# Optimization experiments

Hardware: AMD Instinct MI355X
Metric: run time of the kernel (lower is better)

The kernel has to match this reference:

```python
import jax, jax.numpy as jnp
import numpy as np

N, E, D, H = 100000, 600000, 128, 256
BN_EPS = 1e-5


def setup_inputs() -> dict:
    key = jax.random.key(0)
    ks = jax.random.split(key, 6)
    node_rep = jax.random.normal(ks[0], (N, D), dtype=jnp.float32)
    edge_attr = jax.random.normal(ks[1], (E, D), dtype=jnp.float32)
    src = jax.random.randint(ks[2], (E,), 0, N)
    dst = jax.random.randint(ks[3], (E,), 0, N)
    ones_e = jnp.ones((E,), dtype=jnp.float32)
    degree = jax.ops.segment_sum(ones_e, src, num_segments=N) + \
             jax.ops.segment_sum(ones_e, dst, num_segments=N)
    eps = jnp.zeros((1,), dtype=jnp.float32)
    W1 = jax.random.normal(ks[4], (H, D), dtype=jnp.float32) * 0.05
    W2 = jax.random.normal(ks[5], (D, H), dtype=jnp.float32) * 0.05
    g1 = jnp.ones((H,), dtype=jnp.float32)
    b1 = jnp.zeros((H,), dtype=jnp.float32)
    g2 = jnp.ones((D,), dtype=jnp.float32)
    b2 = jnp.zeros((D,), dtype=jnp.float32)
    return {"node_rep": node_rep, "edge_attr": edge_attr, "degree": degree,
            "eps": eps, "W1": W1, "g1": g1, "b1": b1,
            "W2": W2, "g2": g2, "b2": b2, "src": src, "dst": dst}


def _bn_relu(x, gamma, beta):
    # BatchNorm1d training mode: batch mean, biased variance
    mu = jnp.mean(x, axis=0)
    var = jnp.mean(jnp.square(x - mu), axis=0)
    return jax.nn.relu((x - mu) * jax.lax.rsqrt(var + BN_EPS) * gamma + beta)


def reference(node_rep, edge_attr, degree, eps, W1, g1, b1, W2, g2, b2, src, dst):
    n = node_rep.shape[0]
    # gather nodes -> edges (sum of two endpoint features), add edge attributes
    m = node_rep[src] + node_rep[dst] + edge_attr            # [E, D]
    # gather edges -> nodes (sum over incident edges)
    node_new = jax.ops.segment_sum(m, src, num_segments=n) + \
               jax.ops.segment_sum(m, dst, num_segments=n)  # [N, D]
    # degree-scaled residual: node_new + (1 + eps - deg) * node_rep
    h = node_new + (1.0 + eps - degree[:, None]) * node_rep  # [N, D]
    # 2-layer MLP: Linear(no bias) -> BN -> ReLU, twice
    h = _bn_relu(jnp.einsum('nd,hd->nh', h, W1), g1, b1)     # [N, H]
    out = _bn_relu(jnp.einsum('nh,dh->nd', h, W2), g2, b2)   # [N, D]
    return out
```

## Files before the change

kernel.cpp:

```cpp
#include <hip/hip_runtime.h>
#include <stdint.h>

#define D 128
#define H 256
#define LSTR 264

typedef short s8v __attribute__((ext_vector_type(8)));
typedef float f4v __attribute__((ext_vector_type(4)));

__device__ __forceinline__ short f2bf(float f){
  union { float f; unsigned u; } v; v.f = f;
  unsigned r = v.u + 0x7fffu + ((v.u >> 16) & 1u);
  return (short)(r >> 16);
}

__global__ void k_prep(const float* __restrict__ W1, const float* __restrict__ W2,
                       short* __restrict__ W1s, short* __restrict__ W2s,
                       float* __restrict__ st1, float* __restrict__ st2,
                       int* __restrict__ counts, int N_){
  int t = blockIdx.x*256 + threadIdx.x;
  if (t < 32768){
    int j = t & 7, lane = (t>>3) & 63, kt = (t>>9) & 3, jt = t>>11;
    int col = jt*16 + (lane & 15);
    int k   = kt*32 + (lane>>4)*8 + j;
    W1s[t] = f2bf(W1[col*D + k]);
  } else if (t < 65536){
    int u = t - 32768;
    int j = u & 7, lane = (u>>3) & 63, kt = (u>>9) & 7, jt = u>>12;
    int col = jt*16 + (lane & 15);
    int k   = kt*32 + (lane>>4)*8 + j;
    W2s[u] = f2bf(W2[col*H + k]);
  } else if (t < 90112){
    int u = t - 65536;
    if (u < 32*2*H) st1[u] = 0.f;
    else st2[u - 32*2*H] = 0.f;
  } else {
    int u = t - 90112;
    if (u <= N_) counts[u] = 0;
  }
}

__global__ void k_count(const int* __restrict__ src, const int* __restrict__ dst,
                        int* __restrict__ counts, int E_){
  int e = blockIdx.x*256 + threadIdx.x;
  if (e >= E_) return;
  atomicAdd(&counts[src[e]], 1);
  atomicAdd(&counts[dst[e]], 1);
}

__global__ void k_scanA(const int* __restrict__ counts, int* __restrict__ blockSums, int N_){
  int t = threadIdx.x;
  int base = blockIdx.x*1024 + t*4;
  int s = 0;
  if (base + 3 < N_){
    int4 v = *(const int4*)(counts + base);
    s = v.x + v.y + v.z + v.w;
  } else {
    for (int i=0;i<4;i++) if (base+i < N_) s += counts[base+i];
  }
  __shared__ int ws4[4];
  for (int o=1; o<64; o<<=1) s += __shfl_xor(s, o);
  if ((t & 63) == 0) ws4[t>>6] = s;
  __syncthreads();
  if (t == 0) blockSums[blockIdx.x] = ws4[0]+ws4[1]+ws4[2]+ws4[3];
}

__global__ void k_scanB(const int* __restrict__ blockSums, int* __restrict__ blockBase,
                        int* __restrict__ offsets, int nb, int N_){
  __shared__ int part[1024];
  int t = threadIdx.x;
  int v = (t < nb) ? blockSums[t] : 0;
  part[t] = v;
  __syncthreads();
  for (int o=1; o<1024; o<<=1){
    int u = (t >= o) ? part[t-o] : 0;
    __syncthreads();
    part[t] += u;
    __syncthreads();
  }
  if (t < nb) blockBase[t] = part[t] - v;
  if (t == nb-1) offsets[N_] = part[t];
}

__global__ void k_scanC(const int* __restrict__ counts, const int* __restrict__ blockBase,
                        int* __restrict__ offsets, int* __restrict__ cursor, int N_){
  __shared__ int part[256];
  int t = threadIdx.x;
  int base = blockIdx.x*1024 + t*4;
  int c[4]; int s = 0;
#pragma unroll
  for (int i=0;i<4;i++){ c[i] = (base+i < N_) ? counts[base+i] : 0; s += c[i]; }
  part[t] = s;
  __syncthreads();
  for (int o=1; o<256; o<<=1){
    int u = (t >= o) ? part[t-o] : 0;
    __syncthreads();
    part[t] += u;
    __syncthreads();
  }
  int pos = blockBase[blockIdx.x] + part[t] - s;
#pragma unroll
  for (int i=0;i<4;i++){
    if (base+i < N_){ offsets[base+i] = pos; cursor[base+i] = pos; pos += c[i]; }
  }
}

__global__ void k_fill(const int* __restrict__ src, const int* __restrict__ dst,
                       int* __restrict__ cursor, int* __restrict__ entries, int E_){
  int e = blockIdx.x*256 + threadIdx.x;
  if (e >= E_) return;
  int p = atomicAdd(&cursor[src[e]], 1);
  entries[p] = (e<<1) | 1;
  int q = atomicAdd(&cursor[dst[e]], 1);
  entries[q] = (e<<1);
}

__global__ void k_gather(const float* __restrict__ x, const float* __restrict__ ea,
                         const int* __restrict__ src, const int* __restrict__ dst,
                         const int* __restrict__ offsets, const int* __restrict__ entries,
                         const float* __restrict__ eps, float* __restrict__ h, int N_){
  int n = (blockIdx.x*256 + threadIdx.x) >> 6;
  int lane = threadIdx.x & 63;
  if (n >= N_) return;
  int lo = offsets[n], hi = offsets[n+1];
  float2 xr = ((const float2*)(x + (size_t)n*D))[lane];
  float sc = 1.0f + eps[0];
  float ax = sc*xr.x, ay = sc*xr.y;
  for (int base = lo; base < hi; base += 64){
    int cnt = min(64, hi - base);
    int ent = 0, oth = 0;
    if (lane < cnt){
      ent = entries[base + lane];
      int e = ent >> 1;
      oth = (ent & 1) ? dst[e] : src[e];
    }
    int j = 0;
    for (; j+3 < cnt; j += 4){
      int e0 = __shfl(ent, j)   >> 1, o0 = __shfl(oth, j);
      int e1 = __shfl(ent, j+1) >> 1, o1 = __shfl(oth, j+1);
      int e2 = __shfl(ent, j+2) >> 1, o2 = __shfl(oth, j+2);
      int e3 = __shfl(ent, j+3) >> 1, o3 = __shfl(oth, j+3);
      float2 m0 = ((const float2*)(ea + (size_t)e0*D))[lane];
      float2 x0 = ((const float2*)(x  + (size_t)o0*D))[lane];
      float2 m1 = ((const float2*)(ea + (size_t)e1*D))[lane];
      float2 x1 = ((const float2*)(x  + (size_t)o1*D))[lane];
      float2 m2 = ((const float2*)(ea + (size_t)e2*D))[lane];
      float2 x2 = ((const float2*)(x  + (size_t)o2*D))[lane];
      float2 m3 = ((const float2*)(ea + (size_t)e3*D))[lane];
      float2 x3 = ((const float2*)(x  + (size_t)o3*D))[lane];
      ax += (m0.x + x0.x) + (m1.x + x1.x) + (m2.x + x2.x) + (m3.x + x3.x);
      ay += (m0.y + x0.y) + (m1.y + x1.y) + (m2.y + x2.y) + (m3.y + x3.y);
    }
    for (; j < cnt; j++){
      int e0 = __shfl(ent, j) >> 1, o0 = __shfl(oth, j);
      float2 m0 = ((const float2*)(ea + (size_t)e0*D))[lane];
      float2 x0 = ((const float2*)(x  + (size_t)o0*D))[lane];
      ax += m0.x + x0.x;
      ay += m0.y + x0.y;
    }
  }
  float2 o; o.x = ax; o.y = ay;
  ((float2*)(h + (size_t)n*D))[lane] = o;
}

__global__ void k_gemm1(const float* __restrict__ h, const short* __restrict__ W1s,
                        float* __restrict__ st1, int nW){
  int wid = (blockIdx.x*256 + threadIdx.x) >> 6;
  int lane = threadIdx.x & 63;
  if (wid >= nW) return;
  int r0 = wid*16;
  int mrow = lane & 15, kg = lane >> 4;
  const float* hrow = h + (size_t)(r0 + mrow)*D + kg*8;
  s8v af[4];
#pragma unroll
  for (int kt=0; kt<4; kt++){
    float4 v0 = *(const float4*)(hrow + kt*32);
    float4 v1 = *(const float4*)(hrow + kt*32 + 4);
    s8v a;
    a[0]=f2bf(v0.x); a[1]=f2bf(v0.y); a[2]=f2bf(v0.z); a[3]=f2bf(v0.w);
    a[4]=f2bf(v1.x); a[5]=f2bf(v1.y); a[6]=f2bf(v1.z); a[7]=f2bf(v1.w);
    af[kt] = a;
  }
  const s8v* Bf = (const s8v*)W1s;
  int shadow = wid & 31;
#pragma unroll
  for (int jt=0; jt<16; jt++){
    f4v acc = {0.f,0.f,0.f,0.f};
#pragma unroll
    for (int kt=0; kt<4; kt++)
      acc = __builtin_amdgcn_mfma_f32_16x16x32_bf16(af[kt], Bf[(jt*4+kt)*64 + lane], acc, 0, 0, 0);
    float s = 0.f, q = 0.f;
#pragma unroll
    for (int r=0; r<4; r++){ s += acc[r]; q += acc[r]*acc[r]; }
    s += __shfl_xor(s, 16); s += __shfl_xor(s, 32);
    q += __shfl_xor(q, 16); q += __shfl_xor(q, 32);
    if (lane < 16){
      atomicAdd(&st1[shadow*(2*H) + jt*16 + lane], s);
      atomicAdd(&st1[shadow*(2*H) + H + jt*16 + lane], q);
    }
  }
}

__global__ void k_fin1(const float* __restrict__ st1, const float* __restrict__ g,
                       const float* __restrict__ b, float* __restrict__ a,
                       float* __restrict__ c, float invN){
  int j = threadIdx.x;
  float s=0.f, q=0.f;
  for (int i=0;i<32;i++){ s += st1[i*(2*H) + j]; q += st1[i*(2*H) + H + j]; }
  float mu = s*invN;
  float var = q*invN - mu*mu;
  float rs = rsqrtf(var + 1e-5f);
  float aa = g[j]*rs;
  a[j] = aa; c[j] = b[j] - mu*aa;
}

__launch_bounds__(256)
__global__ void k_gemm2(const float* __restrict__ h, const short* __restrict__ W1s,
                        const short* __restrict__ W2s,
                        const float* __restrict__ a1, const float* __restrict__ c1,
                        float* __restrict__ Y2, float* __restrict__ st2, int nW){
  __shared__ short P[4*16*LSTR];
  int wib  = threadIdx.x >> 6;
  int lane = threadIdx.x & 63;
  int wid  = blockIdx.x*4 + wib;
  bool valid = wid < nW;
  int r0 = wid*16;
  int mrow = lane & 15, kg = lane >> 4;
  short* Pw = P + wib*16*LSTR;

  s8v af[4];
#pragma unroll
  for (int kt=0; kt<4; kt++){ s8v z = {0,0,0,0,0,0,0,0}; af[kt] = z; }
  if (valid){
    const float* hrow = h + (size_t)(r0 + mrow)*D + kg*8;
#pragma unroll
    for (int kt=0; kt<4; kt++){
      float4 v0 = *(const float4*)(hrow + kt*32);
      float4 v1 = *(const float4*)(hrow + kt*32 + 4);
      s8v a;
      a[0]=f2bf(v0.x); a[1]=f2bf(v0.y); a[2]=f2bf(v0.z); a[3]=f2bf(v0.w);
      a[4]=f2bf(v1.x); a[5]=f2bf(v1.y); a[6]=f2bf(v1.z); a[7]=f2bf(v1.w);
      af[kt] = a;
    }
  }

  const s8v* B1 = (const s8v*)W1s;
#pragma unroll
  for (int jt=0; jt<16; jt++){
    f4v acc = {0.f,0.f,0.f,0.f};
#pragma unroll
    for (int kt=0; kt<4; kt++)
      acc = __builtin_amdgcn_mfma_f32_16x16x32_bf16(af[kt], B1[(jt*4+kt)*64 + lane], acc, 0, 0, 0);
    int col = jt*16 + mrow;
    float a = a1[col], c = c1[col];
#pragma unroll
    for (int r=0; r<4; r++){
      float e = fmaxf(acc[r]*a + c, 0.f);
      Pw[(kg*4 + r)*LSTR + col] = f2bf(e);
    }
  }
  __syncthreads();

  s8v af2[8];
#pragma unroll
  for (int kt2=0; kt2<8; kt2++)
    af2[kt2] = *(const s8v*)(Pw + mrow*LSTR + kt2*32 + kg*8);

  const s8v* B2 = (const s8v*)W2s;
  int shadow = wid & 31;
#pragma unroll
  for (int jt=0; jt<8; jt++){
    f4v acc = {0.f,0.f,0.f,0.f};
#pragma unroll
    for (int kt2=0; kt2<8; kt2++)
      acc = __builtin_amdgcn_mfma_f32_16x16x32_bf16(af2[kt2], B2[(jt*8+kt2)*64 + lane], acc, 0, 0, 0);
    float s=0.f, q=0.f;
    if (valid){
#pragma unroll
      for (int r=0; r<4; r++){
        int row = r0 + kg*4 + r;
        Y2[(size_t)row*D + jt*16 + mrow] = acc[r];
        s += acc[r]; q += acc[r]*acc[r];
      }
    }
    s += __shfl_xor(s,16); s += __shfl_xor(s,32);
    q += __shfl_xor(q,16); q += __shfl_xor(q,32);
    if (valid && lane < 16){
      atomicAdd(&st2[shadow*(2*D) + jt*16 + lane], s);
      atomicAdd(&st2[shadow*(2*D) + D + jt*16 + lane], q);
    }
  }
}

__global__ void k_fin2(const float* __restrict__ st2, const float* __restrict__ g,
                       const float* __restrict__ b, float* __restrict__ a,
                       float* __restrict__ c, float invN){
  int j = threadIdx.x;
  float s=0.f, q=0.f;
  for (int i=0;i<32;i++){ s += st2[i*(2*D) + j]; q += st2[i*(2*D) + D + j]; }
  float mu = s*invN;
  float var = q*invN - mu*mu;
  float rs = rsqrtf(var + 1e-5f);
  float aa = g[j]*rs;
  a[j] = aa; c[j] = b[j] - mu*aa;
}

__global__ void k_final(const float* __restrict__ Y2, const float* __restrict__ a2,
                        const float* __restrict__ c2, float* __restrict__ out, int total4){
  int t = blockIdx.x*256 + threadIdx.x;
  if (t >= total4) return;
  int d4 = t & 31;
  float4 v = ((const float4*)Y2)[t];
  float4 A = ((const float4*)a2)[d4];
  float4 C = ((const float4*)c2)[d4];
  float4 o;
  o.x = fmaxf(v.x*A.x + C.x, 0.f);
  o.y = fmaxf(v.y*A.y + C.y, 0.f);
  o.z = fmaxf(v.z*A.z + C.z, 0.f);
  o.w = fmaxf(v.w*A.w + C.w, 0.f);
  ((float4*)out)[t] = o;
}

extern "C" void kernel_launch(void* const* d_in, const int* in_sizes, int n_in,
                              void* d_out, int out_size, void* d_ws, size_t ws_size,
                              hipStream_t stream){
  const float* x   = (const float*)d_in[0];
  const float* ea  = (const float*)d_in[1];
  const float* eps = (const float*)d_in[3];
  const float* W1  = (const float*)d_in[4];
  const float* g1  = (const float*)d_in[5];
  const float* b1  = (const float*)d_in[6];
  const float* W2  = (const float*)d_in[7];
  const float* g2  = (const float*)d_in[8];
  const float* b2  = (const float*)d_in[9];
  const int* src   = (const int*)d_in[10];
  const int* dst   = (const int*)d_in[11];
  float* out = (float*)d_out;

  int N = in_sizes[2];
  int E = in_sizes[10];

  char* w = (char*)d_ws;
  size_t off = 0;
  short* W1s = (short*)(w + off); off += (size_t)H*D*2;
  short* W2s = (short*)(w + off); off += (size_t)D*H*2;
  float* st1 = (float*)(w + off); off += 32*2*H*4;
  float* st2 = (float*)(w + off); off += 32*2*D*4;
  float* a1  = (float*)(w + off); off += H*4;
  float* c1  = (float*)(w + off); off += H*4;
  float* a2  = (float*)(w + off); off += D*4;
  float* c2  = (float*)(w + off); off += D*4;
  int* counts  = (int*)(w + off); off += (size_t)(N+1)*4;
  int* offsets = (int*)(w + off); off += (size_t)(N+1)*4;
  int* cursor  = (int*)(w + off); off += (size_t)N*4;
  int* blockSums = (int*)(w + off); off += 1024*4;
  int* blockBase = (int*)(w + off); off += 1024*4;
  int* entries = (int*)(w + off); off += (size_t)2*E*4;

  float* h = out;

  int prepT = 90112 + N + 1;
  hipLaunchKernelGGL(k_prep, dim3((prepT+255)/256), dim3(256), 0, stream,
                     W1, W2, W1s, W2s, st1, st2, counts, N);
  int eb = (E + 255)/256;
  hipLaunchKernelGGL(k_count, dim3(eb), dim3(256), 0, stream, src, dst, counts, E);
  int nb = (N + 1023)/1024;
  hipLaunchKernelGGL(k_scanA, dim3(nb), dim3(256), 0, stream, counts, blockSums, N);
  hipLaunchKernelGGL(k_scanB, dim3(1), dim3(1024), 0, stream, blockSums, blockBase, offsets, nb, N);
  hipLaunchKernelGGL(k_scanC, dim3(nb), dim3(256), 0, stream, counts, blockBase, offsets, cursor, N);
  hipLaunchKernelGGL(k_fill, dim3(eb), dim3(256), 0, stream, src, dst, cursor, entries, E);
  hipLaunchKernelGGL(k_gather, dim3((N+3)/4), dim3(256), 0, stream,
                     x, ea, src, dst, offsets, entries, eps, h, N);
  int nW = (N + 15)/16;
  int gb = (nW + 3)/4;
  hipLaunchKernelGGL(k_gemm1, dim3(gb), dim3(256), 0, stream, h, W1s, st1, nW);
  hipLaunchKernelGGL(k_fin1, dim3(1), dim3(H), 0, stream, st1, g1, b1, a1, c1, 1.0f/(float)N);
  hipLaunchKernelGGL(k_gemm2, dim3(gb), dim3(256), 0, stream, h, W1s, W2s, a1, c1, h, st2, nW);
  hipLaunchKernelGGL(k_fin2, dim3(1), dim3(D), 0, stream, st2, g2, b2, a2, c2, 1.0f/(float)N);
  int total4 = N*(D/4);
  hipLaunchKernelGGL(k_final, dim3((total4+255)/256), dim3(256), 0, stream, h, a2, c2, out, total4);
}
```

Baseline: 849.9 us.

## Replace CSR build and per-node gather with direct atomic scatter of edge messages

The count, scan and fill kernels that built a CSR adjacency, and the per-node gather, are removed. h is now initialised to (1+eps-deg)*x, and each edge adds its message x[src]+x[dst]+ea to both endpoints with float atomics. This uses the provided degree to fold in the self-endpoint terms, which saves the sort passes and the recomputation of edge values. In exchange it adds 4 float atomics per lane per edge into a 51 MB buffer, and the summation order is no longer deterministic.

```diff
diff --git a/kernel.cpp b/kernel.cpp
--- a/kernel.cpp
+++ b/kernel.cpp
@@ -16,8 +16,7 @@
 
 __global__ void k_prep(const float* __restrict__ W1, const float* __restrict__ W2,
                        short* __restrict__ W1s, short* __restrict__ W2s,
-                       float* __restrict__ st1, float* __restrict__ st2,
-                       int* __restrict__ counts, int N_){
+                       float* __restrict__ st1, float* __restrict__ st2){
   int t = blockIdx.x*256 + threadIdx.x;
   if (t < 32768){
     int j = t & 7, lane = (t>>3) & 63, kt = (t>>9) & 3, jt = t>>11;
@@ -34,133 +33,38 @@
     int u = t - 65536;
     if (u < 32*2*H) st1[u] = 0.f;
     else st2[u - 32*2*H] = 0.f;
-  } else {
-    int u = t - 90112;
-    if (u <= N_) counts[u] = 0;
-  }
-}
-
-__global__ void k_count(const int* __restrict__ src, const int* __restrict__ dst,
-                        int* __restrict__ counts, int E_){
-  int e = blockIdx.x*256 + threadIdx.x;
+  }
+}
+
+__global__ void k_init(const float* __restrict__ x, const float* __restrict__ deg,
+                       const float* __restrict__ eps, float* __restrict__ h, int total4){
+  int t = blockIdx.x*256 + threadIdx.x;
+  if (t >= total4) return;
+  int n = t >> 5;
+  float sc = 1.0f + eps[0] - deg[n];
+  float4 v = ((const float4*)x)[t];
+  v.x *= sc; v.y *= sc; v.z *= sc; v.w *= sc;
+  ((float4*)h)[t] = v;
+}
+
+__global__ void k_scatter(const float* __restrict__ x, const float* __restrict__ ea,
+                          const int* __restrict__ src, const int* __restrict__ dst,
+                          float* __restrict__ h, int E_){
+  int e = blockIdx.x*4 + (threadIdx.x >> 6);
   if (e >= E_) return;
-  atomicAdd(&counts[src[e]], 1);
-  atomicAdd(&counts[dst[e]], 1);
-}
-
-__global__ void k_scanA(const int* __restrict__ counts, int* __restrict__ blockSums, int N_){
-  int t = threadIdx.x;
-  int base = blockIdx.x*1024 + t*4;
-  int s = 0;
-  if (base + 3 < N_){
-    int4 v = *(const int4*)(counts + base);
-    s = v.x + v.y + v.z + v.w;
-  } else {
-    for (int i=0;i<4;i++) if (base+i < N_) s += counts[base+i];
-  }
-  __shared__ int ws4[4];
-  for (int o=1; o<64; o<<=1) s += __shfl_xor(s, o);
-  if ((t & 63) == 0) ws4[t>>6] = s;
-  __syncthreads();
-  if (t == 0) blockSums[blockIdx.x] = ws4[0]+ws4[1]+ws4[2]+ws4[3];
-}
-
-__global__ void k_scanB(const int* __restrict__ blockSums, int* __restrict__ blockBase,
-                        int* __restrict__ offsets, int nb, int N_){
-  __shared__ int part[1024];
-  int t = threadIdx.x;
-  int v = (t < nb) ? blockSums[t] : 0;
-  part[t] = v;
-  __syncthreads();
-  for (int o=1; o<1024; o<<=1){
-    int u = (t >= o) ? part[t-o] : 0;
-    __syncthreads();
-    part[t] += u;
-    __syncthreads();
-  }
-  if (t < nb) blockBase[t] = part[t] - v;
-  if (t == nb-1) offsets[N_] = part[t];
-}
-
-__global__ void k_scanC(const int* __restrict__ counts, const int* __restrict__ blockBase,
-                        int* __restrict__ offsets, int* __restrict__ cursor, int N_){
-  __shared__ int part[256];
-  int t = threadIdx.x;
-  int base = blockIdx.x*1024 + t*4;
-  int c[4]; int s = 0;
-#pragma unroll
-  for (int i=0;i<4;i++){ c[i] = (base+i < N_) ? counts[base+i] : 0; s += c[i]; }
-  part[t] = s;
-  __syncthreads();
-  for (int o=1; o<256; o<<=1){
-    int u = (t >= o) ? part[t-o] : 0;
-    __syncthreads();
-    part[t] += u;
-    __syncthreads();
-  }
-  int pos = blockBase[blockIdx.x] + part[t] - s;
-#pragma unroll
-  for (int i=0;i<4;i++){
-    if (base+i < N_){ offsets[base+i] = pos; cursor[base+i] = pos; pos += c[i]; }
-  }
-}
-
-__global__ void k_fill(const int* __restrict__ src, const int* __restrict__ dst,
-                       int* __restrict__ cursor, int* __restrict__ entries, int E_){
-  int e = blockIdx.x*256 + threadIdx.x;
-  if (e >= E_) return;
-  int p = atomicAdd(&cursor[src[e]], 1);
-  entries[p] = (e<<1) | 1;
-  int q = atomicAdd(&cursor[dst[e]], 1);
-  entries[q] = (e<<1);
-}
-
-__global__ void k_gather(const float* __restrict__ x, const float* __restrict__ ea,
-                         const int* __restrict__ src, const int* __restrict__ dst,
-                         const int* __restrict__ offsets, const int* __restrict__ entries,
-                         const float* __restrict__ eps, float* __restrict__ h, int N_){
-  int n = (blockIdx.x*256 + threadIdx.x) >> 6;
   int lane = threadIdx.x & 63;
-  if (n >= N_) return;
-  int lo = offsets[n], hi = offsets[n+1];
-  float2 xr = ((const float2*)(x + (size_t)n*D))[lane];
-  float sc = 1.0f + eps[0];
-  float ax = sc*xr.x, ay = sc*xr.y;
-  for (int base = lo; base < hi; base += 64){
-    int cnt = min(64, hi - base);
-    int ent = 0, oth = 0;
-    if (lane < cnt){
-      ent = entries[base + lane];
-      int e = ent >> 1;
-      oth = (ent & 1) ? dst[e] : src[e];
-    }
-    int j = 0;
-    for (; j+3 < cnt; j += 4){
-      int e0 = __shfl(ent, j)   >> 1, o0 = __shfl(oth, j);
-      int e1 = __shfl(ent, j+1) >> 1, o1 = __shfl(oth, j+1);
-      int e2 = __shfl(ent, j+2) >> 1, o2 = __shfl(oth, j+2);
-      int e3 = __shfl(ent, j+3) >> 1, o3 = __shfl(oth, j+3);
-      float2 m0 = ((const float2*)(ea + (size_t)e0*D))[lane];
-      float2 x0 = ((const float2*)(x  + (size_t)o0*D))[lane];
-      float2 m1 = ((const float2*)(ea + (size_t)e1*D))[lane];
-      float2 x1 = ((const float2*)(x  + (size_t)o1*D))[lane];
-      float2 m2 = ((const float2*)(ea + (size_t)e2*D))[lane];
-      float2 x2 = ((const float2*)(x  + (size_t)o2*D))[lane];
-      float2 m3 = ((const float2*)(ea + (size_t)e3*D))[lane];
-      float2 x3 = ((const float2*)(x  + (size_t)o3*D))[lane];
-      ax += (m0.x + x0.x) + (m1.x + x1.x) + (m2.x + x2.x) + (m3.x + x3.x);
-      ay += (m0.y + x0.y) + (m1.y + x1.y) + (m2.y + x2.y) + (m3.y + x3.y);
-    }
-    for (; j < cnt; j++){
-      int e0 = __shfl(ent, j) >> 1, o0 = __shfl(oth, j);
-      float2 m0 = ((const float2*)(ea + (size_t)e0*D))[lane];
-      float2 x0 = ((const float2*)(x  + (size_t)o0*D))[lane];
-      ax += m0.x + x0.x;
-      ay += m0.y + x0.y;
-    }
-  }
-  float2 o; o.x = ax; o.y = ay;
-  ((float2*)(h + (size_t)n*D))[lane] = o;
+  int s = src[e], d = dst[e];
+  float2 me = ((const float2*)(ea + (size_t)e*D))[lane];
+  float2 xs = ((const float2*)(x  + (size_t)s*D))[lane];
+  float2 xd = ((const float2*)(x  + (size_t)d*D))[lane];
+  float mx = me.x + xs.x + xd.x;
+  float my = me.y + xs.y + xd.y;
+  float* hs = h + (size_t)s*D + lane*2;
+  float* hd = h + (size_t)d*D + lane*2;
+  atomicAdd(hs,     mx);
+  atomicAdd(hs + 1, my);
+  atomicAdd(hd,     mx);
+  atomicAdd(hd + 1, my);
 }
 
 __global__ void k_gemm1(const float* __restrict__ h, const short* __restrict__ W1s,
@@ -326,6 +230,7 @@
                               hipStream_t stream){
   const float* x   = (const float*)d_in[0];
   const float* ea  = (const float*)d_in[1];
+  const float* deg = (const float*)d_in[2];
   const float* eps = (const float*)d_in[3];
   const float* W1  = (const float*)d_in[4];
   const float* g1  = (const float*)d_in[5];
@@ -350,33 +255,21 @@
   float* c1  = (float*)(w + off); off += H*4;
   float* a2  = (float*)(w + off); off += D*4;
   float* c2  = (float*)(w + off); off += D*4;
-  int* counts  = (int*)(w + off); off += (size_t)(N+1)*4;
-  int* offsets = (int*)(w + off); off += (size_t)(N+1)*4;
-  int* cursor  = (int*)(w + off); off += (size_t)N*4;
-  int* blockSums = (int*)(w + off); off += 1024*4;
-  int* blockBase = (int*)(w + off); off += 1024*4;
-  int* entries = (int*)(w + off); off += (size_t)2*E*4;
 
   float* h = out;
 
-  int prepT = 90112 + N + 1;
-  hipLaunchKernelGGL(k_prep, dim3((prepT+255)/256), dim3(256), 0, stream,
-                     W1, W2, W1s, W2s, st1, st2, counts, N);
-  int eb = (E + 255)/256;
-  hipLaunchKernelGGL(k_count, dim3(eb), dim3(256), 0, stream, src, dst, counts, E);
-  int nb = (N + 1023)/1024;
-  hipLaunchKernelGGL(k_scanA, dim3(nb), dim3(256), 0, stream, counts, blockSums, N);
-  hipLaunchKernelGGL(k_scanB, dim3(1), dim3(1024), 0, stream, blockSums, blockBase, offsets, nb, N);
-  hipLaunchKernelGGL(k_scanC, dim3(nb), dim3(256), 0, stream, counts, blockBase, offsets, cursor, N);
-  hipLaunchKernelGGL(k_fill, dim3(eb), dim3(256), 0, stream, src, dst, cursor, entries, E);
-  hipLaunchKernelGGL(k_gather, dim3((N+3)/4), dim3(256), 0, stream,
-                     x, ea, src, dst, offsets, entries, eps, h, N);
+  hipLaunchKernelGGL(k_prep, dim3(352), dim3(256), 0, stream,
+                     W1, W2, W1s, W2s, st1, st2);
+  int total4 = N*(D/4);
+  hipLaunchKernelGGL(k_init, dim3((total4+255)/256), dim3(256), 0, stream,
+                     x, deg, eps, h, total4);
+  hipLaunchKernelGGL(k_scatter, dim3((E+3)/4), dim3(256), 0, stream,
+                     x, ea, src, dst, h, E);
   int nW = (N + 15)/16;
   int gb = (nW + 3)/4;
   hipLaunchKernelGGL(k_gemm1, dim3(gb), dim3(256), 0, stream, h, W1s, st1, nW);
   hipLaunchKernelGGL(k_fin1, dim3(1), dim3(H), 0, stream, st1, g1, b1, a1, c1, 1.0f/(float)N);
   hipLaunchKernelGGL(k_gemm2, dim3(gb), dim3(256), 0, stream, h, W1s, W2s, a1, c1, h, st2, nW);
   hipLaunchKernelGGL(k_fin2, dim3(1), dim3(D), 0, stream, st2, g2, b2, a2, c2, 1.0f/(float)N);
-  int total4 = N*(D/4);
   hipLaunchKernelGGL(k_final, dim3((total4+255)/256), dim3(256), 0, stream, h, a2, c2, out, total4);
 }
```

After: 1.478 ms. 73.9% more time.
